# Optimization experiments

Hardware: AMD Instinct MI355X
Metric: run time of the kernel (lower is better)

Reference implementation:

```python
import jax, jax.numpy as jnp
import numpy as np

B, T, C, H = 2, 64, 384, 768
LR, MOM, DECAY = 0.01, 0.9, 0.001


def pscan(gates, tokens):
    """parallel_scan_log: x[t] = gates[t]*x[t-1] + tokens[t] along axis 1.
    gates [B,S], tokens [B,S,...]."""
    extra = tokens.ndim - gates.ndim
    g = gates.reshape(gates.shape + (1,) * extra)
    g = jnp.clip(g, 1e-7, 1.0 - 1e-7)
    lc = jnp.cumsum(jnp.log(g), axis=1)              # log cumulative gates
    return jnp.exp(lc) * jnp.cumsum(tokens * jnp.exp(-lc), axis=1)


def setup_inputs():
    key = jax.random.key(0)
    ks = jax.random.split(key, 12)
    s = 0.02
    W0 = jax.random.normal(ks[0], (H, C), jnp.float32) * s
    W1 = jax.random.normal(ks[1], (C, H), jnp.float32) * s
    return {
        "x": jax.random.normal(ks[2], (B, T, C), jnp.float32),
        "Wq": jax.random.normal(ks[3], (C, C), jnp.float32) * s, "bq": jnp.zeros((C,), jnp.float32),
        "Wk": jax.random.normal(ks[4], (C, C), jnp.float32) * s, "bk": jnp.zeros((C,), jnp.float32),
        "Wv": jax.random.normal(ks[5], (C, C), jnp.float32) * s, "bv": jnp.zeros((C,), jnp.float32),
        "Wo": jax.random.normal(ks[6], (C, C), jnp.float32) * s, "bo": jnp.zeros((C,), jnp.float32),
        "init_query": jax.random.normal(ks[7], (1, 1, C), jnp.float32) * s,
        "sW0": jnp.broadcast_to(W0, (B, H, C)) + 0.0,
        "sb0": jnp.zeros((B, H), jnp.float32),
        "sW1": jnp.broadcast_to(W1, (B, C, H)) + 0.0,
        "sb1": jnp.zeros((B, C), jnp.float32),
    }


def reference(x, Wq, bq, Wk, bk, Wv, bv, Wo, bo, init_query, sW0, sb0, sW1, sb1):
    dt = x.dtype
    # ---- retrieval (causal: uses init_query since no previous segment) ----
    q = jnp.broadcast_to(init_query, (B, 1, C)) @ Wq.T + bq          # [B,1,C]
    h_pre = jnp.einsum('bqc,bhc->bqh', q, sW0) + sb0[:, None]
    h = h_pre * jax.nn.sigmoid(h_pre)                                 # SiLU
    pred = jnp.einsum('bqh,bch->bqc', h, sW1) + sb1[:, None]
    out = pred @ Wo.T + bo                                            # [B,1,C]

    # ---- test-time memory update: per-token MSE gradients ----
    k = x @ Wk.T + bk                                                 # [B,T,C]
    v = x @ Wv.T + bv
    h1_pre = jnp.einsum('btc,bhc->bth', k, sW0) + sb0[:, None]
    sig = jax.nn.sigmoid(h1_pre)
    h1 = h1_pre * sig
    p = jnp.einsum('bth,bch->btc', h1, sW1) + sb1[:, None]
    dp = p - v                                                        # d(MSE)/d(pred)
    dW1 = jnp.einsum('btc,bth->btch', dp, h1)                         # [B,T,C,H]
    db1 = dp
    dh1 = jnp.einsum('btc,bch->bth', dp, sW1)
    dh1p = dh1 * (sig * (1 + h1_pre * (1 - sig)))                     # SiLU grad
    dW0 = jnp.einsum('bth,btc->bthc', dh1p, k)                        # [B,T,H,C]
    db0 = dh1p

    # ---- momentum scan + decayed weight scan ----
    def update(W, g):
        surprise = -LR * g                                            # [B,T,...]
        m = pscan(jnp.full((B, T), MOM, dt), (1.0 - MOM) * surprise)  # EMA of surprises
        toks = jnp.concatenate([W[:, None], m], axis=1)               # seed with current weight
        gts = jnp.concatenate([jnp.ones((B, 1), dt),
                               jnp.full((B, T), 1.0 - DECAY, dt)], axis=1)
        return pscan(gts, toks)[:, -1]                                # final weight after segment

    nW0 = update(sW0, dW0)
    nb0 = update(sb0, db0)
    nW1 = update(sW1, dW1)
    nb1 = update(sb1, db1)
    return out, nW0, nb0, nW1, nb1
```

## Files before the change

kernel.cpp:

```cpp
#include <hip/hip_runtime.h>
#include <hip/hip_bf16.h>
#include <cmath>

#define BB 2
#define TT 64
#define CC 384
#define HH 768

#define O_OUT 0
#define O_NW0 768
#define O_NB0 (768 + 589824)
#define O_NW1 (O_NB0 + 1536)
#define O_NB1 (O_NW1 + 589824)

struct Coefs { float ct[TT]; float dfac; };

typedef __attribute__((ext_vector_type(8))) short bf16x8;
typedef __attribute__((ext_vector_type(4))) float f32x4;

__device__ __forceinline__ float bf2f(unsigned short u) {
    union { unsigned int i; float f; } x; x.i = ((unsigned int)u) << 16; return x.f;
}
__device__ __forceinline__ unsigned short f2bf(float f) {
    union { float f; unsigned int i; } u; u.f = f;
    unsigned int x = u.i;
    unsigned int r = (x + 0x7fffu + ((x >> 16) & 1u)) >> 16;
    return (unsigned short)r;
}
__device__ __forceinline__ f32x4 mfma16(bf16x8 a, bf16x8 b, f32x4 c) {
    return __builtin_amdgcn_mfma_f32_16x16x32_bf16(a, b, c, 0, 0, 0);
}
__device__ __forceinline__ bf16x8 ldbf8(const unsigned short* p) {
    return *(const bf16x8*)p;
}
__device__ __forceinline__ bf16x8 ldcvt8(const float* p) {
    float4 a = *(const float4*)p, b = *(const float4*)(p + 4);
    bf16x8 r;
    r[0] = (short)f2bf(a.x); r[1] = (short)f2bf(a.y); r[2] = (short)f2bf(a.z); r[3] = (short)f2bf(a.w);
    r[4] = (short)f2bf(b.x); r[5] = (short)f2bf(b.y); r[6] = (short)f2bf(b.z); r[7] = (short)f2bf(b.w);
    return r;
}
__device__ __forceinline__ bf16x8 ldcvt8s(const float* p, int stride) {
    bf16x8 r;
    #pragma unroll
    for (int i = 0; i < 8; ++i) r[i] = (short)f2bf(p[(size_t)i * stride]);
    return r;
}

__global__ void k_qkv(const float* __restrict__ x,
                      const float* __restrict__ Wk, const float* __restrict__ bk,
                      const float* __restrict__ Wv, const float* __restrict__ bv,
                      const float* __restrict__ Wq, const float* __restrict__ bq,
                      const float* __restrict__ iq,
                      unsigned short* __restrict__ kb_bf, float* __restrict__ vb,
                      float* __restrict__ qb) {
    __shared__ float smem[1024 + 16 * 17];
    const int blk = blockIdx.x, j = threadIdx.x;
    if (blk < 24) {
        const int wid = j >> 6, L = j & 63;
        const int w = blk * 4 + wid;
        const int mp = w % 4, np = w / 4;
        const int lrow = L & 15, kq = (L >> 4) * 8;
        const float* A0 = x + (size_t)(mp * 32 + lrow) * CC;
        const float* A1 = A0 + 16 * CC;
        const int n0 = (2 * np) * 16 + lrow, n1 = n0 + 16;
        const float* B0 = (n0 < CC) ? (Wk + (size_t)n0 * CC) : (Wv + (size_t)(n0 - CC) * CC);
        const float* B1 = (n1 < CC) ? (Wk + (size_t)n1 * CC) : (Wv + (size_t)(n1 - CC) * CC);
        f32x4 acc00 = {0,0,0,0}, acc01 = {0,0,0,0}, acc10 = {0,0,0,0}, acc11 = {0,0,0,0};
        #pragma unroll 2
        for (int s = 0; s < CC / 32; ++s) {
            int k = s * 32 + kq;
            bf16x8 a0 = ldcvt8(A0 + k), a1 = ldcvt8(A1 + k);
            bf16x8 b0 = ldcvt8(B0 + k), b1 = ldcvt8(B1 + k);
            acc00 = mfma16(a0, b0, acc00); acc01 = mfma16(a0, b1, acc01);
            acc10 = mfma16(a1, b0, acc10); acc11 = mfma16(a1, b1, acc11);
        }
        const int quad = L >> 4;
        #pragma unroll
        for (int mi = 0; mi < 2; ++mi) {
            #pragma unroll
            for (int ni = 0; ni < 2; ++ni) {
                f32x4 acc = mi == 0 ? (ni == 0 ? acc00 : acc01) : (ni == 0 ? acc10 : acc11);
                int n = (2 * np + ni) * 16 + lrow;
                #pragma unroll
                for (int r = 0; r < 4; ++r) {
                    int m = mp * 32 + mi * 16 + quad * 4 + r;
                    float v = acc[r];
                    if (n < CC) kb_bf[(size_t)m * CC + n] = f2bf(v + bk[n]);
                    else        vb[(size_t)m * CC + (n - CC)] = v + bv[n - CC];
                }
            }
        }
    } else {
        if (j < CC / 4) ((float4*)smem)[j] = ((const float4*)iq)[j];
        __syncthreads();
        const int nt = blk - 24;
        const int nl = j & 15, ks = j >> 4;
        const int n = nt * 16 + nl;
        const float4* wr = (const float4*)(Wq + (size_t)n * CC + ks * 24);
        float s = 0.f;
        #pragma unroll
        for (int i = 0; i < 6; ++i) {
            float4 a = wr[i];
            const float* v = smem + ks * 24 + i * 4;
            s += a.x * v[0] + a.y * v[1] + a.z * v[2] + a.w * v[3];
        }
        smem[1024 + ks * 17 + nl] = s;
        __syncthreads();
        if (j < 16) {
            float acc = bq[nt * 16 + j];
            #pragma unroll
            for (int kk = 0; kk < 16; ++kk) acc += smem[1024 + kk * 17 + j];
            qb[nt * 16 + j] = acc;
        }
    }
}

__global__ void k_h1(const unsigned short* __restrict__ kb_bf, const float* __restrict__ qb,
                     const float* __restrict__ sW0, const float* __restrict__ sb0,
                     unsigned short* __restrict__ h1_bf, float* __restrict__ dsil,
                     float* __restrict__ hret) {
    __shared__ float smem[1024 + 16 * 17];
    const int blk = blockIdx.x, j = threadIdx.x;
    if (blk < 24) {
        const int b = blk / 12;
        const int wid = j >> 6, L = j & 63;
        const int w = (blk % 12) * 4 + wid;
        const int mp = w & 1, np = w >> 1;
        const int lrow = L & 15, kq = (L >> 4) * 8;
        const unsigned short* A0 = kb_bf + (size_t)(b * TT + mp * 32 + lrow) * CC;
        const unsigned short* A1 = A0 + 16 * CC;
        const int n0 = (2 * np) * 16 + lrow;
        const float* B0 = sW0 + (size_t)(b * HH + n0) * CC;
        const float* B1 = B0 + 16 * CC;
        f32x4 acc00 = {0,0,0,0}, acc01 = {0,0,0,0}, acc10 = {0,0,0,0}, acc11 = {0,0,0,0};
        #pragma unroll 2
        for (int s = 0; s < CC / 32; ++s) {
            int k = s * 32 + kq;
            bf16x8 a0 = ldbf8(A0 + k), a1 = ldbf8(A1 + k);
            bf16x8 b0 = ldcvt8(B0 + k), b1 = ldcvt8(B1 + k);
            acc00 = mfma16(a0, b0, acc00); acc01 = mfma16(a0, b1, acc01);
            acc10 = mfma16(a1, b0, acc10); acc11 = mfma16(a1, b1, acc11);
        }
        const int quad = L >> 4;
        #pragma unroll
        for (int mi = 0; mi < 2; ++mi) {
            #pragma unroll
            for (int ni = 0; ni < 2; ++ni) {
                f32x4 acc = mi == 0 ? (ni == 0 ? acc00 : acc01) : (ni == 0 ? acc10 : acc11);
                int n = (2 * np + ni) * 16 + lrow;
                float bias = sb0[b * HH + n];
                #pragma unroll
                for (int r = 0; r < 4; ++r) {
                    int t = mp * 32 + mi * 16 + quad * 4 + r;
                    float pre = acc[r] + bias;
                    float sig = 1.f / (1.f + expf(-pre));
                    size_t idx = (size_t)(b * TT + t) * HH + n;
                    h1_bf[idx] = f2bf(pre * sig);
                    dsil[idx]  = sig * (1.f + pre * (1.f - sig));
                }
            }
        }
    } else {
        if (j < CC / 4) ((float4*)smem)[j] = ((const float4*)qb)[j];
        __syncthreads();
        const int rb = blk - 24;
        const int b = rb / 48, nt = rb % 48;
        const int nl = j & 15, ks = j >> 4;
        const int n = nt * 16 + nl;
        const float4* wr = (const float4*)(sW0 + (size_t)(b * HH + n) * CC + ks * 24);
        float s = 0.f;
        #pragma unroll
        for (int i = 0; i < 6; ++i) {
            float4 a = wr[i];
            const float* v = smem + ks * 24 + i * 4;
            s += a.x * v[0] + a.y * v[1] + a.z * v[2] + a.w * v[3];
        }
        smem[1024 + ks * 17 + nl] = s;
        __syncthreads();
        if (j < 16) {
            int n2 = nt * 16 + j;
            float pre = sb0[b * HH + n2];
            #pragma unroll
            for (int kk = 0; kk < 16; ++kk) pre += smem[1024 + kk * 17 + j];
            float sig = 1.f / (1.f + expf(-pre));
            hret[b * HH + n2] = pre * sig;
        }
    }
}

__global__ void k_p(const unsigned short* __restrict__ h1_bf, const float* __restrict__ hret,
                    const float* __restrict__ vb,
                    const float* __restrict__ sW1, const float* __restrict__ sb1,
                    unsigned short* __restrict__ dp_bf, float* __restrict__ pred) {
    __shared__ float smem[1024 + 16 * 17];
    const int blk = blockIdx.x, j = threadIdx.x;
    if (blk < 12) {
        const int b = blk / 6;
        const int wid = j >> 6, L = j & 63;
        const int w = (blk % 6) * 4 + wid;
        const int mp = w & 1, np = w >> 1;
        const int lrow = L & 15, kq = (L >> 4) * 8;
        const unsigned short* A0 = h1_bf + (size_t)(b * TT + mp * 32 + lrow) * HH;
        const unsigned short* A1 = A0 + 16 * HH;
        const int n0 = (2 * np) * 16 + lrow;
        const float* B0 = sW1 + (size_t)(b * CC + n0) * HH;
        const float* B1 = B0 + 16 * HH;
        f32x4 acc00 = {0,0,0,0}, acc01 = {0,0,0,0}, acc10 = {0,0,0,0}, acc11 = {0,0,0,0};
        #pragma unroll 2
        for (int s = 0; s < HH / 32; ++s) {
            int k = s * 32 + kq;
            bf16x8 a0 = ldbf8(A0 + k), a1 = ldbf8(A1 + k);
            bf16x8 b0 = ldcvt8(B0 + k), b1 = ldcvt8(B1 + k);
            acc00 = mfma16(a0, b0, acc00); acc01 = mfma16(a0, b1, acc01);
            acc10 = mfma16(a1, b0, acc10); acc11 = mfma16(a1, b1, acc11);
        }
        const int quad = L >> 4;
        #pragma unroll
        for (int mi = 0; mi < 2; ++mi) {
            #pragma unroll
            for (int ni = 0; ni < 2; ++ni) {
                f32x4 acc = mi == 0 ? (ni == 0 ? acc00 : acc01) : (ni == 0 ? acc10 : acc11);
                int n = (2 * np + ni) * 16 + lrow;
                float bias = sb1[b * CC + n];
                #pragma unroll
                for (int r = 0; r < 4; ++r) {
                    int t = mp * 32 + mi * 16 + quad * 4 + r;
                    size_t idx = (size_t)(b * TT + t) * CC + n;
                    dp_bf[idx] = f2bf(acc[r] + bias - vb[idx]);
                }
            }
        }
    } else {
        const int rb = blk - 12;
        const int b = rb / 24, nt = rb % 24;
        if (j < HH / 4) ((float4*)smem)[j] = ((const float4*)(hret + b * HH))[j];
        __syncthreads();
        const int nl = j & 15, ks = j >> 4;
        const int n = nt * 16 + nl;
        const float4* wr = (const float4*)(sW1 + (size_t)(b * CC + n) * HH + ks * 48);
        float s = 0.f;
        #pragma unroll
        for (int i = 0; i < 12; ++i) {
            float4 a = wr[i];
            const float* v = smem + ks * 48 + i * 4;
            s += a.x * v[0] + a.y * v[1] + a.z * v[2] + a.w * v[3];
        }
        smem[1024 + ks * 17 + nl] = s;
        __syncthreads();
        if (j < 16) {
            int n2 = nt * 16 + j;
            float acc = sb1[b * CC + n2];
            #pragma unroll
            for (int kk = 0; kk < 16; ++kk) acc += smem[1024 + kk * 17 + j];
            pred[b * CC + n2] = acc;
        }
    }
}

__global__ void k_epi1(const unsigned short* __restrict__ dp_bf,
                       const unsigned short* __restrict__ h1_bf,
                       const float* __restrict__ dsil,
                       const float* __restrict__ sW1, const float* __restrict__ sb1,
                       const float* __restrict__ pred,
                       const float* __restrict__ Wo, const float* __restrict__ bo,
                       unsigned short* __restrict__ dh1p_bf,
                       float* __restrict__ out, Coefs cf) {
    __shared__ float smem[6144];
    const int blk = blockIdx.x, j = threadIdx.x;
    if (blk < 24) {
        const int b = blk / 12;
        const int wid = j >> 6, L = j & 63;
        const int w = (blk % 12) * 4 + wid;
        const int mp = w & 1, np = w >> 1;
        const int lrow = L & 15, kq = (L >> 4) * 8;
        const unsigned short* A0 = dp_bf + (size_t)(b * TT + mp * 32 + lrow) * CC;
        const unsigned short* A1 = A0 + 16 * CC;
        const int n0 = (2 * np) * 16 + lrow, n1 = n0 + 16;
        const float* Bb = sW1 + (size_t)b * CC * HH;
        f32x4 acc00 = {0,0,0,0}, acc01 = {0,0,0,0}, acc10 = {0,0,0,0}, acc11 = {0,0,0,0};
        for (int s = 0; s < CC / 32; ++s) {
            int k = s * 32 + kq;
            bf16x8 a0 = ldbf8(A0 + k), a1 = ldbf8(A1 + k);
            bf16x8 b0 = ldcvt8s(Bb + (size_t)k * HH + n0, HH);
            bf16x8 b1 = ldcvt8s(Bb + (size_t)k * HH + n1, HH);
            acc00 = mfma16(a0, b0, acc00); acc01 = mfma16(a0, b1, acc01);
            acc10 = mfma16(a1, b0, acc10); acc11 = mfma16(a1, b1, acc11);
        }
        const int quad = L >> 4;
        #pragma unroll
        for (int mi = 0; mi < 2; ++mi) {
            #pragma unroll
            for (int ni = 0; ni < 2; ++ni) {
                f32x4 acc = mi == 0 ? (ni == 0 ? acc00 : acc01) : (ni == 0 ? acc10 : acc11);
                int n = (2 * np + ni) * 16 + lrow;
                #pragma unroll
                for (int r = 0; r < 4; ++r) {
                    int t = mp * 32 + mi * 16 + quad * 4 + r;
                    size_t idx = (size_t)(b * TT + t) * HH + n;
                    dh1p_bf[idx] = f2bf(acc[r] * dsil[idx]);
                }
            }
        }
    } else if (blk < 312) {
        float* a_t = smem;
        float* e_t = smem + 2048;
        const int u = blk - 24;
        const int b = u / 144, rem = u % 144;
        const int c0 = (rem / 12) * 32, h0 = (rem % 12) * 64;
        for (int i = j; i < TT * 32; i += 256) {
            int t = i >> 5, c = i & 31;
            a_t[t * 32 + c] = cf.ct[t] * bf2f(dp_bf[((size_t)(b * TT + t)) * CC + c0 + c]);
        }
        for (int i = j; i < TT * 64; i += 256) {
            int t = i >> 6, h = i & 63;
            e_t[t * 64 + h] = bf2f(h1_bf[((size_t)(b * TT + t)) * HH + h0 + h]);
        }
        __syncthreads();
        const int ci = j & 31, hb = (j >> 5) * 8;
        float acc[8] = {0, 0, 0, 0, 0, 0, 0, 0};
        for (int t = 0; t < TT; ++t) {
            float av = a_t[t * 32 + ci];
            #pragma unroll
            for (int m = 0; m < 8; ++m) acc[m] += av * e_t[t * 64 + hb + m];
        }
        const size_t idx = ((size_t)b * CC + c0 + ci) * HH + h0 + hb;
        const float4* w4 = (const float4*)(sW1 + idx);
        float4 wa = w4[0], wb = w4[1];
        float4 o0, o1;
        o0.x = cf.dfac * wa.x - acc[0]; o0.y = cf.dfac * wa.y - acc[1];
        o0.z = cf.dfac * wa.z - acc[2]; o0.w = cf.dfac * wa.w - acc[3];
        o1.x = cf.dfac * wb.x - acc[4]; o1.y = cf.dfac * wb.y - acc[5];
        o1.z = cf.dfac * wb.z - acc[6]; o1.w = cf.dfac * wb.w - acc[7];
        *(float4*)(out + O_NW1 + idx) = o0;
        *(float4*)(out + O_NW1 + idx + 4) = o1;
        if (h0 == 0 && j < 32) {
            float s = 0.f;
            for (int t = 0; t < TT; ++t) s += a_t[t * 32 + j];
            out[O_NB1 + b * CC + c0 + j] = cf.dfac * sb1[b * CC + c0 + j] - s;
        }
    } else {
        const int rb = blk - 312;
        const int b = rb / 24, nt = rb % 24;
        if (j < CC / 4) ((float4*)smem)[j] = ((const float4*)(pred + b * CC))[j];
        __syncthreads();
        const int nl = j & 15, ks = j >> 4;
        const int n = nt * 16 + nl;
        const float4* wr = (const float4*)(Wo + (size_t)n * CC + ks * 24);
        float s = 0.f;
        #pragma unroll
        for (int i = 0; i < 6; ++i) {
            float4 a = wr[i];
            const float* v = smem + ks * 24 + i * 4;
            s += a.x * v[0] + a.y * v[1] + a.z * v[2] + a.w * v[3];
        }
        smem[1024 + ks * 17 + nl] = s;
        __syncthreads();
        if (j < 16) {
            int n2 = nt * 16 + j;
            float acc = bo[n2];
            #pragma unroll
            for (int kk = 0; kk < 16; ++kk) acc += smem[1024 + kk * 17 + j];
            out[O_OUT + b * CC + n2] = acc;
        }
    }
}

__global__ void k_epi2(const unsigned short* __restrict__ dh1p_bf,
                       const unsigned short* __restrict__ kb_bf,
                       const float* __restrict__ sW0, const float* __restrict__ sb0,
                       float* __restrict__ out, Coefs cf) {
    __shared__ float smem[6144];
    float* a_t = smem;
    float* e_t = smem + 2048;
    const int blk = blockIdx.x, j = threadIdx.x;
    const int b = blk / 144, rem = blk % 144;
    const int h0 = (rem / 6) * 32, c0 = (rem % 6) * 64;
    for (int i = j; i < TT * 32; i += 256) {
        int t = i >> 5, h = i & 31;
        a_t[t * 32 + h] = cf.ct[t] * bf2f(dh1p_bf[((size_t)(b * TT + t)) * HH + h0 + h]);
    }
    for (int i = j; i < TT * 64; i += 256) {
        int t = i >> 6, c = i & 63;
        e_t[t * 64 + c] = bf2f(kb_bf[((size_t)(b * TT + t)) * CC + c0 + c]);
    }
    __syncthreads();
    const int hi = j & 31, cb = (j >> 5) * 8;
    float acc[8] = {0, 0, 0, 0, 0, 0, 0, 0};
    for (int t = 0; t < TT; ++t) {
        float av = a_t[t * 32 + hi];
        #pragma unroll
        for (int m = 0; m < 8; ++m) acc[m] += av * e_t[t * 64 + cb + m];
    }
    const size_t idx = ((size_t)b * HH + h0 + hi) * CC + c0 + cb;
    const float4* w4 = (const float4*)(sW0 + idx);
    float4 wa = w4[0], wb = w4[1];
    float4 o0, o1;
    o0.x = cf.dfac * wa.x - acc[0]; o0.y = cf.dfac * wa.y - acc[1];
    o0.z = cf.dfac * wa.z - acc[2]; o0.w = cf.dfac * wa.w - acc[3];
    o1.x = cf.dfac * wb.x - acc[4]; o1.y = cf.dfac * wb.y - acc[5];
    o1.z = cf.dfac * wb.z - acc[6]; o1.w = cf.dfac * wb.w - acc[7];
    *(float4*)(out + O_NW0 + idx) = o0;
    *(float4*)(out + O_NW0 + idx + 4) = o1;
    if (c0 == 0 && j < 32) {
        float s = 0.f;
        for (int t = 0; t < TT; ++t) s += a_t[t * 32 + j];
        out[O_NB0 + b * HH + h0 + j] = cf.dfac * sb0[b * HH + h0 + j] - s;
    }
}

extern "C" void kernel_launch(void* const* d_in, const int* in_sizes, int n_in,
                              void* d_out, int out_size, void* d_ws, size_t ws_size,
                              hipStream_t stream) {
    const float* x   = (const float*)d_in[0];
    const float* Wq  = (const float*)d_in[1];
    const float* bq  = (const float*)d_in[2];
    const float* Wk  = (const float*)d_in[3];
    const float* bk  = (const float*)d_in[4];
    const float* Wv  = (const float*)d_in[5];
    const float* bv  = (const float*)d_in[6];
    const float* Wo  = (const float*)d_in[7];
    const float* bo  = (const float*)d_in[8];
    const float* iq  = (const float*)d_in[9];
    const float* sW0 = (const float*)d_in[10];
    const float* sb0 = (const float*)d_in[11];
    const float* sW1 = (const float*)d_in[12];
    const float* sb1 = (const float*)d_in[13];

    float* fw = (float*)d_ws;
    float* qb   = fw;
    float* hret = qb + 384;
    float* pred = hret + 1536;
    float* vb   = pred + 768;
    float* dsil = vb + 49152;
    unsigned short* us = (unsigned short*)(dsil + 98304);
    unsigned short* kb_bf   = us;
    unsigned short* h1_bf   = kb_bf + 49152;
    unsigned short* dp_bf   = h1_bf + 98304;
    unsigned short* dh1p_bf = dp_bf + 49152;

    Coefs cf;
    const double mom = 0.9, decay = 1.0 - 0.001, lr = 0.01;
    for (int s = 0; s < TT; ++s) {
        double sum = 0.0;
        for (int t = s; t < TT; ++t) sum += pow(decay, (double)(TT - 1 - t)) * pow(mom, (double)(t - s));
        cf.ct[s] = (float)(lr * (1.0 - mom) * sum);
    }
    cf.dfac = (float)pow(decay, (double)TT);

    k_qkv <<<dim3(48),  dim3(256), 0, stream>>>(x, Wk, bk, Wv, bv, Wq, bq, iq, kb_bf, vb, qb);
    k_h1  <<<dim3(120), dim3(256), 0, stream>>>(kb_bf, qb, sW0, sb0, h1_bf, dsil, hret);
    k_p   <<<dim3(60),  dim3(256), 0, stream>>>(h1_bf, hret, vb, sW1, sb1, dp_bf, pred);
    k_epi1<<<dim3(360), dim3(256), 0, stream>>>(dp_bf, h1_bf, dsil, sW1, sb1, pred, Wo, bo,
                                                dh1p_bf, (float*)d_out, cf);
    k_epi2<<<dim3(288), dim3(256), 0, stream>>>(dh1p_bf, kb_bf, sW0, sb0, (float*)d_out, cf);
}
```

Measured before the change: 145.8 us.

## Fold single-row query GEMVs into MFMA waves and shrink per-wave tiles

The separate GEMV block paths for q, retrieval hidden and pred are replaced by an extra MFMA wave per column pair that treats the single query row as a padded 16-row tile. Per-wave tiles shrink from 32x32 to 16x32 and the grid layouts are reworked to match. This removes the shared-memory GEMV branches and the barriers they need, and spreads the same work over more waves. In exchange, the query waves compute 15 wasted rows, and the smaller tiles reload each B operand for every 16-row fragment, which raises global traffic.

```diff
diff --git a/kernel.cpp b/kernel.cpp
--- a/kernel.cpp
+++ b/kernel.cpp
@@ -47,265 +47,206 @@
     return r;
 }
 
-__global__ void k_qkv(const float* __restrict__ x,
-                      const float* __restrict__ Wk, const float* __restrict__ bk,
-                      const float* __restrict__ Wv, const float* __restrict__ bv,
-                      const float* __restrict__ Wq, const float* __restrict__ bq,
-                      const float* __restrict__ iq,
-                      unsigned short* __restrict__ kb_bf, float* __restrict__ vb,
-                      float* __restrict__ qb) {
-    __shared__ float smem[1024 + 16 * 17];
-    const int blk = blockIdx.x, j = threadIdx.x;
-    if (blk < 24) {
-        const int wid = j >> 6, L = j & 63;
-        const int w = blk * 4 + wid;
-        const int mp = w % 4, np = w / 4;
-        const int lrow = L & 15, kq = (L >> 4) * 8;
-        const float* A0 = x + (size_t)(mp * 32 + lrow) * CC;
-        const float* A1 = A0 + 16 * CC;
-        const int n0 = (2 * np) * 16 + lrow, n1 = n0 + 16;
-        const float* B0 = (n0 < CC) ? (Wk + (size_t)n0 * CC) : (Wv + (size_t)(n0 - CC) * CC);
-        const float* B1 = (n1 < CC) ? (Wk + (size_t)n1 * CC) : (Wv + (size_t)(n1 - CC) * CC);
-        f32x4 acc00 = {0,0,0,0}, acc01 = {0,0,0,0}, acc10 = {0,0,0,0}, acc11 = {0,0,0,0};
+__global__ void __launch_bounds__(256) k_qkv(
+        const float* __restrict__ x,
+        const float* __restrict__ Wk, const float* __restrict__ bk,
+        const float* __restrict__ Wv, const float* __restrict__ bv,
+        const float* __restrict__ Wq, const float* __restrict__ bq,
+        const float* __restrict__ iq,
+        unsigned short* __restrict__ kb_bf, float* __restrict__ vb,
+        float* __restrict__ qb) {
+    const int blk = blockIdx.x, j = threadIdx.x;
+    const int wid = j >> 6, L = j & 63;
+    const int w = blk * 4 + wid;
+    const int lrow = L & 15, kq = (L >> 4) * 8, quad = L >> 4;
+    int mf, npair;
+    if (w < 192) { mf = w % 8; npair = w / 8; }
+    else         { mf = 8;     npair = 24 + (w - 192); }
+    const float* Arow = (mf < 8) ? (x + (size_t)(mf * 16 + lrow) * CC) : iq;
+    const int n0 = npair * 32 + lrow, n1 = n0 + 16;
+    const float* B0 = (n0 < CC) ? (Wk + (size_t)n0 * CC)
+                    : (n0 < 2 * CC) ? (Wv + (size_t)(n0 - CC) * CC)
+                    : (Wq + (size_t)(n0 - 2 * CC) * CC);
+    const float* B1 = (n1 < CC) ? (Wk + (size_t)n1 * CC)
+                    : (n1 < 2 * CC) ? (Wv + (size_t)(n1 - CC) * CC)
+                    : (Wq + (size_t)(n1 - 2 * CC) * CC);
+    f32x4 acc0 = {0,0,0,0}, acc1 = {0,0,0,0};
+    #pragma unroll 2
+    for (int s = 0; s < CC / 32; ++s) {
+        int k = s * 32 + kq;
+        bf16x8 a = ldcvt8(Arow + k);
+        bf16x8 b0 = ldcvt8(B0 + k), b1 = ldcvt8(B1 + k);
+        acc0 = mfma16(a, b0, acc0); acc1 = mfma16(a, b1, acc1);
+    }
+    #pragma unroll
+    for (int ni = 0; ni < 2; ++ni) {
+        f32x4 acc = ni == 0 ? acc0 : acc1;
+        int n = npair * 32 + ni * 16 + lrow;
+        if (mf < 8) {
+            #pragma unroll
+            for (int r = 0; r < 4; ++r) {
+                int m = mf * 16 + quad * 4 + r;
+                float v = acc[r];
+                if (n < CC) kb_bf[(size_t)m * CC + n] = f2bf(v + bk[n]);
+                else        vb[(size_t)m * CC + (n - CC)] = v + bv[n - CC];
+            }
+        } else if (quad == 0) {
+            qb[n - 2 * CC] = acc[0] + bq[n - 2 * CC];
+        }
+    }
+}
+
+__global__ void __launch_bounds__(256) k_h1(
+        const unsigned short* __restrict__ kb_bf, const float* __restrict__ qb,
+        const float* __restrict__ sW0, const float* __restrict__ sb0,
+        unsigned short* __restrict__ h1_bf, float* __restrict__ dsil,
+        float* __restrict__ hret) {
+    const int blk = blockIdx.x, j = threadIdx.x;
+    const int b = blk / 30;
+    const int wid = j >> 6, L = j & 63;
+    const int w = (blk % 30) * 4 + wid;
+    const int mf = w % 5, npair = w / 5;
+    const int lrow = L & 15, kq = (L >> 4) * 8, quad = L >> 4;
+    const unsigned short* Abf = kb_bf + (size_t)(b * TT + mf * 16 + lrow) * CC;
+    const int n0 = npair * 32 + lrow;
+    const float* B0 = sW0 + (size_t)(b * HH + n0) * CC;
+    const float* B1 = B0 + 16 * CC;
+    f32x4 acc0 = {0,0,0,0}, acc1 = {0,0,0,0};
+    if (mf < 4) {
         #pragma unroll 2
         for (int s = 0; s < CC / 32; ++s) {
             int k = s * 32 + kq;
-            bf16x8 a0 = ldcvt8(A0 + k), a1 = ldcvt8(A1 + k);
+            bf16x8 a = ldbf8(Abf + k);
             bf16x8 b0 = ldcvt8(B0 + k), b1 = ldcvt8(B1 + k);
-            acc00 = mfma16(a0, b0, acc00); acc01 = mfma16(a0, b1, acc01);
-            acc10 = mfma16(a1, b0, acc10); acc11 = mfma16(a1, b1, acc11);
-        }
-        const int quad = L >> 4;
-        #pragma unroll
-        for (int mi = 0; mi < 2; ++mi) {
-            #pragma unroll
-            for (int ni = 0; ni < 2; ++ni) {
-                f32x4 acc = mi == 0 ? (ni == 0 ? acc00 : acc01) : (ni == 0 ? acc10 : acc11);
-                int n = (2 * np + ni) * 16 + lrow;
-                #pragma unroll
-                for (int r = 0; r < 4; ++r) {
-                    int m = mp * 32 + mi * 16 + quad * 4 + r;
-                    float v = acc[r];
-                    if (n < CC) kb_bf[(size_t)m * CC + n] = f2bf(v + bk[n]);
-                    else        vb[(size_t)m * CC + (n - CC)] = v + bv[n - CC];
-                }
-            }
+            acc0 = mfma16(a, b0, acc0); acc1 = mfma16(a, b1, acc1);
         }
     } else {
-        if (j < CC / 4) ((float4*)smem)[j] = ((const float4*)iq)[j];
-        __syncthreads();
-        const int nt = blk - 24;
-        const int nl = j & 15, ks = j >> 4;
-        const int n = nt * 16 + nl;
-        const float4* wr = (const float4*)(Wq + (size_t)n * CC + ks * 24);
-        float s = 0.f;
-        #pragma unroll
-        for (int i = 0; i < 6; ++i) {
-            float4 a = wr[i];
-            const float* v = smem + ks * 24 + i * 4;
-            s += a.x * v[0] + a.y * v[1] + a.z * v[2] + a.w * v[3];
-        }
-        smem[1024 + ks * 17 + nl] = s;
-        __syncthreads();
-        if (j < 16) {
-            float acc = bq[nt * 16 + j];
-            #pragma unroll
-            for (int kk = 0; kk < 16; ++kk) acc += smem[1024 + kk * 17 + j];
-            qb[nt * 16 + j] = acc;
-        }
-    }
-}
-
-__global__ void k_h1(const unsigned short* __restrict__ kb_bf, const float* __restrict__ qb,
-                     const float* __restrict__ sW0, const float* __restrict__ sb0,
-                     unsigned short* __restrict__ h1_bf, float* __restrict__ dsil,
-                     float* __restrict__ hret) {
-    __shared__ float smem[1024 + 16 * 17];
-    const int blk = blockIdx.x, j = threadIdx.x;
-    if (blk < 24) {
-        const int b = blk / 12;
-        const int wid = j >> 6, L = j & 63;
-        const int w = (blk % 12) * 4 + wid;
-        const int mp = w & 1, np = w >> 1;
-        const int lrow = L & 15, kq = (L >> 4) * 8;
-        const unsigned short* A0 = kb_bf + (size_t)(b * TT + mp * 32 + lrow) * CC;
-        const unsigned short* A1 = A0 + 16 * CC;
-        const int n0 = (2 * np) * 16 + lrow;
-        const float* B0 = sW0 + (size_t)(b * HH + n0) * CC;
-        const float* B1 = B0 + 16 * CC;
-        f32x4 acc00 = {0,0,0,0}, acc01 = {0,0,0,0}, acc10 = {0,0,0,0}, acc11 = {0,0,0,0};
         #pragma unroll 2
         for (int s = 0; s < CC / 32; ++s) {
             int k = s * 32 + kq;
-            bf16x8 a0 = ldbf8(A0 + k), a1 = ldbf8(A1 + k);
+            bf16x8 a = ldcvt8(qb + k);
             bf16x8 b0 = ldcvt8(B0 + k), b1 = ldcvt8(B1 + k);
-            acc00 = mfma16(a0, b0, acc00); acc01 = mfma16(a0, b1, acc01);
-            acc10 = mfma16(a1, b0, acc10); acc11 = mfma16(a1, b1, acc11);
-        }
-        const int quad = L >> 4;
-        #pragma unroll
-        for (int mi = 0; mi < 2; ++mi) {
-            #pragma unroll
-            for (int ni = 0; ni < 2; ++ni) {
-                f32x4 acc = mi == 0 ? (ni == 0 ? acc00 : acc01) : (ni == 0 ? acc10 : acc11);
-                int n = (2 * np + ni) * 16 + lrow;
-                float bias = sb0[b * HH + n];
-                #pragma unroll
-                for (int r = 0; r < 4; ++r) {
-                    int t = mp * 32 + mi * 16 + quad * 4 + r;
-                    float pre = acc[r] + bias;
-                    float sig = 1.f / (1.f + expf(-pre));
-                    size_t idx = (size_t)(b * TT + t) * HH + n;
-                    h1_bf[idx] = f2bf(pre * sig);
-                    dsil[idx]  = sig * (1.f + pre * (1.f - sig));
-                }
+            acc0 = mfma16(a, b0, acc0); acc1 = mfma16(a, b1, acc1);
+        }
+    }
+    #pragma unroll
+    for (int ni = 0; ni < 2; ++ni) {
+        f32x4 acc = ni == 0 ? acc0 : acc1;
+        int n = npair * 32 + ni * 16 + lrow;
+        float bias = sb0[b * HH + n];
+        if (mf < 4) {
+            #pragma unroll
+            for (int r = 0; r < 4; ++r) {
+                int t = mf * 16 + quad * 4 + r;
+                float pre = acc[r] + bias;
+                float sig = 1.f / (1.f + expf(-pre));
+                size_t idx = (size_t)(b * TT + t) * HH + n;
+                h1_bf[idx] = f2bf(pre * sig);
+                dsil[idx]  = sig * (1.f + pre * (1.f - sig));
             }
-        }
-    } else {
-        if (j < CC / 4) ((float4*)smem)[j] = ((const float4*)qb)[j];
-        __syncthreads();
-        const int rb = blk - 24;
-        const int b = rb / 48, nt = rb % 48;
-        const int nl = j & 15, ks = j >> 4;
-        const int n = nt * 16 + nl;
-        const float4* wr = (const float4*)(sW0 + (size_t)(b * HH + n) * CC + ks * 24);
-        float s = 0.f;
-        #pragma unroll
-        for (int i = 0; i < 6; ++i) {
-            float4 a = wr[i];
-            const float* v = smem + ks * 24 + i * 4;
-            s += a.x * v[0] + a.y * v[1] + a.z * v[2] + a.w * v[3];
-        }
-        smem[1024 + ks * 17 + nl] = s;
-        __syncthreads();
-        if (j < 16) {
-            int n2 = nt * 16 + j;
-            float pre = sb0[b * HH + n2];
-            #pragma unroll
-            for (int kk = 0; kk < 16; ++kk) pre += smem[1024 + kk * 17 + j];
+        } else if (quad == 0) {
+            float pre = acc[0] + bias;
             float sig = 1.f / (1.f + expf(-pre));
-            hret[b * HH + n2] = pre * sig;
-        }
-    }
-}
-
-__global__ void k_p(const unsigned short* __restrict__ h1_bf, const float* __restrict__ hret,
-                    const float* __restrict__ vb,
-                    const float* __restrict__ sW1, const float* __restrict__ sb1,
-                    unsigned short* __restrict__ dp_bf, float* __restrict__ pred) {
-    __shared__ float smem[1024 + 16 * 17];
-    const int blk = blockIdx.x, j = threadIdx.x;
-    if (blk < 12) {
-        const int b = blk / 6;
-        const int wid = j >> 6, L = j & 63;
-        const int w = (blk % 6) * 4 + wid;
-        const int mp = w & 1, np = w >> 1;
-        const int lrow = L & 15, kq = (L >> 4) * 8;
-        const unsigned short* A0 = h1_bf + (size_t)(b * TT + mp * 32 + lrow) * HH;
-        const unsigned short* A1 = A0 + 16 * HH;
-        const int n0 = (2 * np) * 16 + lrow;
-        const float* B0 = sW1 + (size_t)(b * CC + n0) * HH;
-        const float* B1 = B0 + 16 * HH;
-        f32x4 acc00 = {0,0,0,0}, acc01 = {0,0,0,0}, acc10 = {0,0,0,0}, acc11 = {0,0,0,0};
+            hret[b * HH + n] = pre * sig;
+        }
+    }
+}
+
+__global__ void __launch_bounds__(256) k_p(
+        const unsigned short* __restrict__ h1_bf, const float* __restrict__ hret,
+        const float* __restrict__ vb,
+        const float* __restrict__ sW1, const float* __restrict__ sb1,
+        unsigned short* __restrict__ dp_bf, float* __restrict__ pred) {
+    const int blk = blockIdx.x, j = threadIdx.x;
+    const int b = blk / 15;
+    const int wid = j >> 6, L = j & 63;
+    const int w = (blk % 15) * 4 + wid;
+    const int mf = w % 5, npair = w / 5;
+    const int lrow = L & 15, kq = (L >> 4) * 8, quad = L >> 4;
+    const unsigned short* Abf = h1_bf + (size_t)(b * TT + mf * 16 + lrow) * HH;
+    const float* Aq = hret + (size_t)b * HH;
+    const int n0 = npair * 32 + lrow;
+    const float* B0 = sW1 + (size_t)(b * CC + n0) * HH;
+    const float* B1 = B0 + 16 * HH;
+    f32x4 acc0 = {0,0,0,0}, acc1 = {0,0,0,0};
+    if (mf < 4) {
         #pragma unroll 2
         for (int s = 0; s < HH / 32; ++s) {
             int k = s * 32 + kq;
-            bf16x8 a0 = ldbf8(A0 + k), a1 = ldbf8(A1 + k);
+            bf16x8 a = ldbf8(Abf + k);
             bf16x8 b0 = ldcvt8(B0 + k), b1 = ldcvt8(B1 + k);
-            acc00 = mfma16(a0, b0, acc00); acc01 = mfma16(a0, b1, acc01);
-            acc10 = mfma16(a1, b0, acc10); acc11 = mfma16(a1, b1, acc11);
-        }
-        const int quad = L >> 4;
-        #pragma unroll
-        for (int mi = 0; mi < 2; ++mi) {
-            #pragma unroll
-            for (int ni = 0; ni < 2; ++ni) {
-                f32x4 acc = mi == 0 ? (ni == 0 ? acc00 : acc01) : (ni == 0 ? acc10 : acc11);
-                int n = (2 * np + ni) * 16 + lrow;
-                float bias = sb1[b * CC + n];
-                #pragma unroll
-                for (int r = 0; r < 4; ++r) {
-                    int t = mp * 32 + mi * 16 + quad * 4 + r;
-                    size_t idx = (size_t)(b * TT + t) * CC + n;
-                    dp_bf[idx] = f2bf(acc[r] + bias - vb[idx]);
-                }
+            acc0 = mfma16(a, b0, acc0); acc1 = mfma16(a, b1, acc1);
+        }
+    } else {
+        #pragma unroll 2
+        for (int s = 0; s < HH / 32; ++s) {
+            int k = s * 32 + kq;
+            bf16x8 a = ldcvt8(Aq + k);
+            bf16x8 b0 = ldcvt8(B0 + k), b1 = ldcvt8(B1 + k);
+            acc0 = mfma16(a, b0, acc0); acc1 = mfma16(a, b1, acc1);
+        }
+    }
+    #pragma unroll
+    for (int ni = 0; ni < 2; ++ni) {
+        f32x4 acc = ni == 0 ? acc0 : acc1;
+        int n = npair * 32 + ni * 16 + lrow;
+        float bias = sb1[b * CC + n];
+        if (mf < 4) {
+            #pragma unroll
+            for (int r = 0; r < 4; ++r) {
+                int t = mf * 16 + quad * 4 + r;
+                size_t idx = (size_t)(b * TT + t) * CC + n;
+                dp_bf[idx] = f2bf(acc[r] + bias - vb[idx]);
             }
-        }
-    } else {
-        const int rb = blk - 12;
-        const int b = rb / 24, nt = rb % 24;
-        if (j < HH / 4) ((float4*)smem)[j] = ((const float4*)(hret + b * HH))[j];
-        __syncthreads();
-        const int nl = j & 15, ks = j >> 4;
-        const int n = nt * 16 + nl;
-        const float4* wr = (const float4*)(sW1 + (size_t)(b * CC + n) * HH + ks * 48);
-        float s = 0.f;
-        #pragma unroll
-        for (int i = 0; i < 12; ++i) {
-            float4 a = wr[i];
-            const float* v = smem + ks * 48 + i * 4;
-            s += a.x * v[0] + a.y * v[1] + a.z * v[2] + a.w * v[3];
-        }
-        smem[1024 + ks * 17 + nl] = s;
-        __syncthreads();
-        if (j < 16) {
-            int n2 = nt * 16 + j;
-            float acc = sb1[b * CC + n2];
-            #pragma unroll
-            for (int kk = 0; kk < 16; ++kk) acc += smem[1024 + kk * 17 + j];
-            pred[b * CC + n2] = acc;
-        }
-    }
-}
-
-__global__ void k_epi1(const unsigned short* __restrict__ dp_bf,
-                       const unsigned short* __restrict__ h1_bf,
-                       const float* __restrict__ dsil,
-                       const float* __restrict__ sW1, const float* __restrict__ sb1,
-                       const float* __restrict__ pred,
-                       const float* __restrict__ Wo, const float* __restrict__ bo,
-                       unsigned short* __restrict__ dh1p_bf,
-                       float* __restrict__ out, Coefs cf) {
+        } else if (quad == 0) {
+            pred[b * CC + n] = acc[0] + bias;
+        }
+    }
+}
+
+__global__ void __launch_bounds__(256) k_epi1(
+        const unsigned short* __restrict__ dp_bf,
+        const unsigned short* __restrict__ h1_bf,
+        const float* __restrict__ dsil,
+        const float* __restrict__ sW1, const float* __restrict__ sb1,
+        const float* __restrict__ pred,
+        const float* __restrict__ Wo, const float* __restrict__ bo,
+        unsigned short* __restrict__ dh1p_bf,
+        float* __restrict__ out, Coefs cf) {
     __shared__ float smem[6144];
     const int blk = blockIdx.x, j = threadIdx.x;
-    if (blk < 24) {
-        const int b = blk / 12;
+    if (blk < 48) {
+        const int b = blk / 24;
         const int wid = j >> 6, L = j & 63;
-        const int w = (blk % 12) * 4 + wid;
-        const int mp = w & 1, np = w >> 1;
-        const int lrow = L & 15, kq = (L >> 4) * 8;
-        const unsigned short* A0 = dp_bf + (size_t)(b * TT + mp * 32 + lrow) * CC;
-        const unsigned short* A1 = A0 + 16 * CC;
-        const int n0 = (2 * np) * 16 + lrow, n1 = n0 + 16;
+        const int w = (blk % 24) * 4 + wid;
+        const int mf = w % 4, npair = w / 4;
+        const int lrow = L & 15, kq = (L >> 4) * 8, quad = L >> 4;
+        const unsigned short* Abf = dp_bf + (size_t)(b * TT + mf * 16 + lrow) * CC;
+        const int n0 = npair * 32 + lrow, n1 = n0 + 16;
         const float* Bb = sW1 + (size_t)b * CC * HH;
-        f32x4 acc00 = {0,0,0,0}, acc01 = {0,0,0,0}, acc10 = {0,0,0,0}, acc11 = {0,0,0,0};
+        f32x4 acc0 = {0,0,0,0}, acc1 = {0,0,0,0};
         for (int s = 0; s < CC / 32; ++s) {
             int k = s * 32 + kq;
-            bf16x8 a0 = ldbf8(A0 + k), a1 = ldbf8(A1 + k);
+            bf16x8 a = ldbf8(Abf + k);
             bf16x8 b0 = ldcvt8s(Bb + (size_t)k * HH + n0, HH);
             bf16x8 b1 = ldcvt8s(Bb + (size_t)k * HH + n1, HH);
-            acc00 = mfma16(a0, b0, acc00); acc01 = mfma16(a0, b1, acc01);
-            acc10 = mfma16(a1, b0, acc10); acc11 = mfma16(a1, b1, acc11);
-        }
-        const int quad = L >> 4;
+            acc0 = mfma16(a, b0, acc0); acc1 = mfma16(a, b1, acc1);
+        }
         #pragma unroll
-        for (int mi = 0; mi < 2; ++mi) {
-            #pragma unroll
-            for (int ni = 0; ni < 2; ++ni) {
-                f32x4 acc = mi == 0 ? (ni == 0 ? acc00 : acc01) : (ni == 0 ? acc10 : acc11);
-                int n = (2 * np + ni) * 16 + lrow;
-                #pragma unroll
-                for (int r = 0; r < 4; ++r) {
-                    int t = mp * 32 + mi * 16 + quad * 4 + r;
-                    size_t idx = (size_t)(b * TT + t) * HH + n;
-                    dh1p_bf[idx] = f2bf(acc[r] * dsil[idx]);
-                }
+        for (int ni = 0; ni < 2; ++ni) {
+            f32x4 acc = ni == 0 ? acc0 : acc1;
+            int n = npair * 32 + ni * 16 + lrow;
+            #pragma unroll
+            for (int r = 0; r < 4; ++r) {
+                int t = mf * 16 + quad * 4 + r;
+                size_t idx = (size_t)(b * TT + t) * HH + n;
+                dh1p_bf[idx] = f2bf(acc[r] * dsil[idx]);
             }
         }
-    } else if (blk < 312) {
+    } else if (blk < 336) {
         float* a_t = smem;
         float* e_t = smem + 2048;
-        const int u = blk - 24;
+        const int u = blk - 48;
         const int b = u / 144, rem = u % 144;
         const int c0 = (rem / 12) * 32, h0 = (rem % 12) * 64;
         for (int i = j; i < TT * 32; i += 256) {
@@ -340,7 +281,7 @@
             out[O_NB1 + b * CC + c0 + j] = cf.dfac * sb1[b * CC + c0 + j] - s;
         }
     } else {
-        const int rb = blk - 312;
+        const int rb = blk - 336;
         const int b = rb / 24, nt = rb % 24;
         if (j < CC / 4) ((float4*)smem)[j] = ((const float4*)(pred + b * CC))[j];
         __syncthreads();
@@ -366,10 +307,11 @@
     }
 }
 
-__global__ void k_epi2(const unsigned short* __restrict__ dh1p_bf,
-                       const unsigned short* __restrict__ kb_bf,
-                       const float* __restrict__ sW0, const float* __restrict__ sb0,
-                       float* __restrict__ out, Coefs cf) {
+__global__ void __launch_bounds__(256) k_epi2(
+        const unsigned short* __restrict__ dh1p_bf,
+        const unsigned short* __restrict__ kb_bf,
+        const float* __restrict__ sW0, const float* __restrict__ sb0,
+        float* __restrict__ out, Coefs cf) {
     __shared__ float smem[6144];
     float* a_t = smem;
     float* e_t = smem + 2048;
@@ -448,10 +390,10 @@
     }
     cf.dfac = (float)pow(decay, (double)TT);
 
-    k_qkv <<<dim3(48),  dim3(256), 0, stream>>>(x, Wk, bk, Wv, bv, Wq, bq, iq, kb_bf, vb, qb);
-    k_h1  <<<dim3(120), dim3(256), 0, stream>>>(kb_bf, qb, sW0, sb0, h1_bf, dsil, hret);
-    k_p   <<<dim3(60),  dim3(256), 0, stream>>>(h1_bf, hret, vb, sW1, sb1, dp_bf, pred);
-    k_epi1<<<dim3(360), dim3(256), 0, stream>>>(dp_bf, h1_bf, dsil, sW1, sb1, pred, Wo, bo,
+    k_qkv <<<dim3(51),  dim3(256), 0, stream>>>(x, Wk, bk, Wv, bv, Wq, bq, iq, kb_bf, vb, qb);
+    k_h1  <<<dim3(60),  dim3(256), 0, stream>>>(kb_bf, qb, sW0, sb0, h1_bf, dsil, hret);
+    k_p   <<<dim3(30),  dim3(256), 0, stream>>>(h1_bf, hret, vb, sW1, sb1, dp_bf, pred);
+    k_epi1<<<dim3(384), dim3(256), 0, stream>>>(dp_bf, h1_bf, dsil, sW1, sb1, pred, Wo, bo,
                                                 dh1p_bf, (float*)d_out, cf);
     k_epi2<<<dim3(288), dim3(256), 0, stream>>>(dh1p_bf, kb_bf, sW0, sb0, (float*)d_out, cf);
 }
```

New measurement: 142.0 us. 1.03x faster.
